# Optimization experiments

Measured on AMD Instinct MI355X. Metric: run time of the kernel, lower is better.

The kernel has to match this reference:

```python
import jax, jax.numpy as jnp
import numpy as np

EPS = 1e-5  # torch LayerNorm default


def setup_inputs() -> dict:
    key = jax.random.key(0)
    ks = jax.random.split(key, 7)
    B, s, i, c, h = 1, 1024, 512, 8, 8
    scale = 0.1
    return {
        "m": jax.random.normal(ks[0], (B, s, i, c), dtype=jnp.float32),
        "ln_gamma": jnp.ones((c,), dtype=jnp.float32),
        "ln_beta": jnp.zeros((c,), dtype=jnp.float32),
        "Wq": jax.random.normal(ks[1], (c * h, c), dtype=jnp.float32) * scale,
        "Wk": jax.random.normal(ks[2], (c, c), dtype=jnp.float32) * scale,
        "Wv": jax.random.normal(ks[3], (c, c), dtype=jnp.float32) * scale,
        "Wg": jax.random.normal(ks[4], (c * h, c), dtype=jnp.float32) * scale,
        "Wo": jax.random.normal(ks[5], (c, c * h), dtype=jnp.float32) * scale,
        "bo": jnp.zeros((c,), dtype=jnp.float32),
    }


def reference(m, ln_gamma, ln_beta, Wq, Wk, Wv, Wg, Wo, bo):
    c = Wk.shape[0]
    h = Wq.shape[0] // c
    B, s, i, _ = m.shape

    # LayerNorm over the channel dim c
    mu = jnp.mean(m, axis=-1, keepdims=True)
    var = jnp.mean(jnp.square(m - mu), axis=-1, keepdims=True)
    x = (m - mu) * jax.lax.rsqrt(var + EPS) * ln_gamma + ln_beta  # (B,s,i,c)

    # projections (torch Linear: y = x @ W.T)
    q = (x @ Wq.T).reshape(B, s, i, h, c).mean(axis=1)            # (B,i,h,c) mean-pooled query
    k = x @ Wk.T                                                   # (B,s,i,c)
    v = x @ Wv.T                                                   # (B,s,i,c)
    gate = jax.nn.sigmoid(x @ Wg.T).reshape(B, s, i, h, c)        # (B,s,i,h,c)

    # attention logits over the column axis t (=s), softmax along t (dim=-3 of b t i h)
    a = jnp.einsum('bihc,btic->btih', q, k) * (c ** -0.5)          # (B,s,i,h)
    a = jax.nn.softmax(a, axis=1)

    o = gate * jnp.einsum('btih,btic->btihc', a, v)               # (B,s,i,h,c)
    o = o.reshape(B, s, i, h * c)
    return o @ Wo.T + bo                                           # (B,s,i,c)
```

## Files before the change

kernel.cpp:

```cpp
#include <hip/hip_runtime.h>

namespace {
constexpr int S = 1024, I = 512, C = 8, H = 8;
constexpr float LNEPS = 1e-5f;
constexpr float SCALE = 0.35355339059327373f;
}

__device__ __forceinline__ float dot8(const float x[8], float4 a, float4 b) {
    float r = x[0] * a.x;
    r += x[1] * a.y; r += x[2] * a.z; r += x[3] * a.w;
    r += x[4] * b.x; r += x[5] * b.y; r += x[6] * b.z; r += x[7] * b.w;
    return r;
}

__device__ __forceinline__ void ln8(float4 a, float4 b, const float gm[8],
                                    const float bt[8], float x[8]) {
    x[0] = a.x; x[1] = a.y; x[2] = a.z; x[3] = a.w;
    x[4] = b.x; x[5] = b.y; x[6] = b.z; x[7] = b.w;
    float mu = 0.f;
#pragma unroll
    for (int c = 0; c < 8; c++) mu += x[c];
    mu *= 0.125f;
    float var = 0.f;
#pragma unroll
    for (int c = 0; c < 8; c++) { float d = x[c] - mu; var += d * d; }
    var *= 0.125f;
    float inv = rsqrtf(var + LNEPS);
#pragma unroll
    for (int c = 0; c < 8; c++) x[c] = (x[c] - mu) * inv * gm[c] + bt[c];
}

__global__ __launch_bounds__(256) void k1_part(const float* __restrict__ m,
                                               const float* __restrict__ gamma,
                                               const float* __restrict__ beta,
                                               float* __restrict__ part1, int CH1) {
    int g = blockIdx.x * 256 + threadIdx.x;
    int i = g & (I - 1);
    int sc = g >> 9;
    int niter = S / CH1;
    float gm[8], bt[8];
#pragma unroll
    for (int c = 0; c < 8; c++) { gm[c] = gamma[c]; bt[c] = beta[c]; }
    float acc[8];
#pragma unroll
    for (int c = 0; c < 8; c++) acc[c] = 0.f;
    const float4* m4 = (const float4*)m;
    for (int j = 0; j < niter; j++) {
        int row = (sc * niter + j) * I + i;
        float x[8];
        ln8(m4[row * 2], m4[row * 2 + 1], gm, bt, x);
#pragma unroll
        for (int c = 0; c < 8; c++) acc[c] += x[c];
    }
    float4* p4 = (float4*)&part1[((size_t)sc * I + i) * 8];
    p4[0] = make_float4(acc[0], acc[1], acc[2], acc[3]);
    p4[1] = make_float4(acc[4], acc[5], acc[6], acc[7]);
}

__global__ __launch_bounds__(64) void k1b_qk(const float* __restrict__ part1,
                                             const float* __restrict__ Wq,
                                             const float* __restrict__ Wk,
                                             float* __restrict__ qk, int CH1) {
    int i = blockIdx.x, t = threadIdx.x;
    float xs[8];
#pragma unroll
    for (int c = 0; c < 8; c++) xs[c] = 0.f;
    const float4* p4 = (const float4*)part1;
    for (int p = t; p < CH1; p += 64) {
        float4 a = p4[((size_t)p * I + i) * 2], b = p4[((size_t)p * I + i) * 2 + 1];
        xs[0] += a.x; xs[1] += a.y; xs[2] += a.z; xs[3] += a.w;
        xs[4] += b.x; xs[5] += b.y; xs[6] += b.z; xs[7] += b.w;
    }
#pragma unroll
    for (int d = 1; d < 64; d <<= 1)
#pragma unroll
        for (int c = 0; c < 8; c++) xs[c] += __shfl_xor(xs[c], d, 64);
    int h = t >> 3, c2 = t & 7;
    float acc = 0.f;
#pragma unroll
    for (int c = 0; c < 8; c++) {
        float qc = 0.f;
#pragma unroll
        for (int c3 = 0; c3 < 8; c3++) qc += xs[c3] * Wq[(h * 8 + c) * 8 + c3];
        acc += qc * Wk[c * 8 + c2];
    }
    qk[i * 64 + t] = acc * (SCALE / 1024.0f);
}

__global__ __launch_bounds__(256) void k2_part(const float* __restrict__ m,
                                               const float* __restrict__ gamma,
                                               const float* __restrict__ beta,
                                               const float* __restrict__ qk,
                                               float* __restrict__ part2, int CH2) {
    int g = blockIdx.x * 256 + threadIdx.x;
    int i = g & (I - 1);
    int sc = g >> 9;
    int niter = S / CH2;
    float gm[8], bt[8];
#pragma unroll
    for (int c = 0; c < 8; c++) { gm[c] = gamma[c]; bt[c] = beta[c]; }
    const float4* qk4 = (const float4*)qk;
    float4 qv[16];
#pragma unroll
    for (int j = 0; j < 16; j++) qv[j] = qk4[i * 16 + j];
    float acc[8];
#pragma unroll
    for (int h = 0; h < 8; h++) acc[h] = 0.f;
    const float4* m4 = (const float4*)m;
    for (int j0 = 0; j0 < niter; j0 += 4) {
        float x[4][8];
#pragma unroll
        for (int r = 0; r < 4; r++) {
            int row = (sc * niter + j0 + r) * I + i;
            ln8(m4[row * 2], m4[row * 2 + 1], gm, bt, x[r]);
        }
#pragma unroll
        for (int h = 0; h < 8; h++)
#pragma unroll
            for (int r = 0; r < 4; r++)
                acc[h] += __expf(dot8(x[r], qv[h * 2], qv[h * 2 + 1]));
    }
    float4* p4 = (float4*)&part2[((size_t)sc * I + i) * 8];
    p4[0] = make_float4(acc[0], acc[1], acc[2], acc[3]);
    p4[1] = make_float4(acc[4], acc[5], acc[6], acc[7]);
}

__global__ __launch_bounds__(64) void k2b_rden(const float* __restrict__ part2,
                                               float* __restrict__ rden, int CH2) {
    int i = blockIdx.x, t = threadIdx.x;
    float d[8];
#pragma unroll
    for (int c = 0; c < 8; c++) d[c] = 0.f;
    const float4* p4 = (const float4*)part2;
    for (int p = t; p < CH2; p += 64) {
        float4 a = p4[((size_t)p * I + i) * 2], b = p4[((size_t)p * I + i) * 2 + 1];
        d[0] += a.x; d[1] += a.y; d[2] += a.z; d[3] += a.w;
        d[4] += b.x; d[5] += b.y; d[6] += b.z; d[7] += b.w;
    }
#pragma unroll
    for (int dd = 1; dd < 64; dd <<= 1)
#pragma unroll
        for (int c = 0; c < 8; c++) d[c] += __shfl_xor(d[c], dd, 64);
    if (t < 8) rden[i * 8 + t] = 1.0f / d[t];
}

__global__ __launch_bounds__(256) void k3_out(const float* __restrict__ m,
                                              const float* __restrict__ gamma,
                                              const float* __restrict__ beta,
                                              const float* __restrict__ Wv,
                                              const float* __restrict__ Wg,
                                              const float* __restrict__ Wo,
                                              const float* __restrict__ bo,
                                              const float* __restrict__ qk,
                                              const float* __restrict__ rden,
                                              float* __restrict__ out) {
    __shared__ __align__(16) float sWv[64];
    __shared__ __align__(16) float sWg[512];
    __shared__ __align__(16) float sWoT[512];
    int t = threadIdx.x;
    if (t < 64) sWv[t] = Wv[t];
    sWg[t] = Wg[t];
    sWg[t + 256] = Wg[t + 256];
    {
        int j = t & 63, c2 = t >> 6;
        sWoT[j * 8 + c2] = Wo[c2 * 64 + j];
        sWoT[j * 8 + c2 + 4] = Wo[(c2 + 4) * 64 + j];
    }
    __syncthreads();

    float gm[8], bt[8], bov[8];
#pragma unroll
    for (int c = 0; c < 8; c++) { gm[c] = gamma[c]; bt[c] = beta[c]; bov[c] = bo[c]; }

    int g = blockIdx.x * 256 + t;
    int i = g & (I - 1);
    int sg = g >> 9;
    const float4* m4 = (const float4*)m;
    float4* out4 = (float4*)out;

    float4 xa[4], xb[4];
#pragma unroll
    for (int r = 0; r < 4; r++) {
        int row = (sg + 256 * r) * I + i;
        xa[r] = m4[row * 2]; xb[r] = m4[row * 2 + 1];
    }
    float x[4][8];
#pragma unroll
    for (int r = 0; r < 4; r++) ln8(xa[r], xb[r], gm, bt, x[r]);

    const float4* sWv4 = (const float4*)sWv;
    const float4* sWg4 = (const float4*)sWg;
    const float4* sWoT4 = (const float4*)sWoT;

    float v[4][8];
#pragma unroll
    for (int c = 0; c < 8; c++) {
        float4 w0 = sWv4[c * 2], w1 = sWv4[c * 2 + 1];
#pragma unroll
        for (int r = 0; r < 4; r++) v[r][c] = dot8(x[r], w0, w1);
    }

    float oacc[4][8];
#pragma unroll
    for (int r = 0; r < 4; r++)
#pragma unroll
        for (int c2 = 0; c2 < 8; c2++) oacc[r][c2] = bov[c2];

    const float4* qk4 = (const float4*)qk;
#pragma unroll 1
    for (int h = 0; h < 8; h++) {
        float4 q0 = qk4[i * 16 + h * 2], q1 = qk4[i * 16 + h * 2 + 1];
        float rd = rden[i * 8 + h];
        float a_[4];
#pragma unroll
        for (int r = 0; r < 4; r++) a_[r] = __expf(dot8(x[r], q0, q1)) * rd;
#pragma unroll
        for (int c = 0; c < 8; c++) {
            int hc = h * 8 + c;
            float4 wg0 = sWg4[hc * 2], wg1 = sWg4[hc * 2 + 1];
            float o_[4];
#pragma unroll
            for (int r = 0; r < 4; r++) {
                float z = dot8(x[r], wg0, wg1);
                float gate = __builtin_amdgcn_rcpf(1.0f + __expf(-z));
                o_[r] = gate * a_[r] * v[r][c];
            }
            float4 wo0 = sWoT4[hc * 2], wo1 = sWoT4[hc * 2 + 1];
#pragma unroll
            for (int r = 0; r < 4; r++) {
                oacc[r][0] += o_[r] * wo0.x; oacc[r][1] += o_[r] * wo0.y;
                oacc[r][2] += o_[r] * wo0.z; oacc[r][3] += o_[r] * wo0.w;
                oacc[r][4] += o_[r] * wo1.x; oacc[r][5] += o_[r] * wo1.y;
                oacc[r][6] += o_[r] * wo1.z; oacc[r][7] += o_[r] * wo1.w;
            }
        }
    }
#pragma unroll
    for (int r = 0; r < 4; r++) {
        int row = (sg + 256 * r) * I + i;
        out4[row * 2] = make_float4(oacc[r][0], oacc[r][1], oacc[r][2], oacc[r][3]);
        out4[row * 2 + 1] = make_float4(oacc[r][4], oacc[r][5], oacc[r][6], oacc[r][7]);
    }
}

extern "C" void kernel_launch(void* const* d_in, const int* in_sizes, int n_in,
                              void* d_out, int out_size, void* d_ws, size_t ws_size,
                              hipStream_t stream) {
    const float* m     = (const float*)d_in[0];
    const float* gamma = (const float*)d_in[1];
    const float* beta  = (const float*)d_in[2];
    const float* Wq    = (const float*)d_in[3];
    const float* Wk    = (const float*)d_in[4];
    const float* Wv    = (const float*)d_in[5];
    const float* Wg    = (const float*)d_in[6];
    const float* Wo    = (const float*)d_in[7];
    const float* bo    = (const float*)d_in[8];
    float* out = (float*)d_out;

    const size_t small = (size_t)I * 64 * 4 + (size_t)I * 8 * 4;
    int CH1 = 256, CH2 = 256;
    auto need = [&](int c1, int c2) {
        return ((size_t)(c1 + c2) * I * C * 4) + small;
    };
    if (need(256, 256) > ws_size) { CH1 = CH2 = 64; }
    if (need(CH1, CH2) > ws_size) { CH1 = CH2 = 16; }

    float* ws    = (float*)d_ws;
    float* part1 = ws;
    float* part2 = part1 + (size_t)CH1 * I * C;
    float* qk    = part2 + (size_t)CH2 * I * C;
    float* rden  = qk + (size_t)I * 64;

    k1_part<<<I * CH1 / 256, 256, 0, stream>>>(m, gamma, beta, part1, CH1);
    k1b_qk<<<I, 64, 0, stream>>>(part1, Wq, Wk, qk, CH1);
    k2_part<<<I * CH2 / 256, 256, 0, stream>>>(m, gamma, beta, qk, part2, CH2);
    k2b_rden<<<I, 64, 0, stream>>>(part2, rden, CH2);
    k3_out<<<I * 256 / 256, 256, 0, stream>>>(m, gamma, beta, Wv, Wg, Wo, bo, qk,
                                              rden, out);
}
```

Baseline: 131.9 us.

## Restructure reductions to coalesced 8-column blocks and double output-kernel grid

The two partial-sum reduction kernels now process 8 columns per 256-thread block. Each wave reads a contiguous 64-float slice per chunk, and the waves combine through shared memory, replacing one 64-thread block per column with strided float4 loads. The output kernel handles 2 rows per thread instead of 4 and launches twice as many blocks with a 4-blocks-per-SM launch bound, aiming for more occupancy and lower register pressure. The chunk count is now a fixed compile-time constant of 256, so the loops fully unroll. The workspace-size fallback is removed, which risks overflow if the workspace is smaller than needed.

```diff
diff --git a/kernel.cpp b/kernel.cpp
--- a/kernel.cpp
+++ b/kernel.cpp
@@ -4,6 +4,7 @@
 constexpr int S = 1024, I = 512, C = 8, H = 8;
 constexpr float LNEPS = 1e-5f;
 constexpr float SCALE = 0.35355339059327373f;
+constexpr int CH = 256;
 }
 
 __device__ __forceinline__ float dot8(const float x[8], float4 a, float4 b) {
@@ -30,14 +31,14 @@
     for (int c = 0; c < 8; c++) x[c] = (x[c] - mu) * inv * gm[c] + bt[c];
 }
 
-__global__ __launch_bounds__(256) void k1_part(const float* __restrict__ m,
-                                               const float* __restrict__ gamma,
-                                               const float* __restrict__ beta,
-                                               float* __restrict__ part1, int CH1) {
+__global__ __launch_bounds__(256) void kA1_part(const float* __restrict__ m,
+                                                const float* __restrict__ gamma,
+                                                const float* __restrict__ beta,
+                                                float* __restrict__ part1) {
     int g = blockIdx.x * 256 + threadIdx.x;
     int i = g & (I - 1);
     int sc = g >> 9;
-    int niter = S / CH1;
+    constexpr int NIT = S / CH;
     float gm[8], bt[8];
 #pragma unroll
     for (int c = 0; c < 8; c++) { gm[c] = gamma[c]; bt[c] = beta[c]; }
@@ -45,8 +46,9 @@
 #pragma unroll
     for (int c = 0; c < 8; c++) acc[c] = 0.f;
     const float4* m4 = (const float4*)m;
-    for (int j = 0; j < niter; j++) {
-        int row = (sc * niter + j) * I + i;
+#pragma unroll
+    for (int j = 0; j < NIT; j++) {
+        int row = (sc * NIT + j) * I + i;
         float x[8];
         ln8(m4[row * 2], m4[row * 2 + 1], gm, bt, x);
 #pragma unroll
@@ -57,45 +59,55 @@
     p4[1] = make_float4(acc[4], acc[5], acc[6], acc[7]);
 }
 
-__global__ __launch_bounds__(64) void k1b_qk(const float* __restrict__ part1,
-                                             const float* __restrict__ Wq,
-                                             const float* __restrict__ Wk,
-                                             float* __restrict__ qk, int CH1) {
-    int i = blockIdx.x, t = threadIdx.x;
-    float xs[8];
-#pragma unroll
-    for (int c = 0; c < 8; c++) xs[c] = 0.f;
-    const float4* p4 = (const float4*)part1;
-    for (int p = t; p < CH1; p += 64) {
-        float4 a = p4[((size_t)p * I + i) * 2], b = p4[((size_t)p * I + i) * 2 + 1];
-        xs[0] += a.x; xs[1] += a.y; xs[2] += a.z; xs[3] += a.w;
-        xs[4] += b.x; xs[5] += b.y; xs[6] += b.z; xs[7] += b.w;
-    }
-#pragma unroll
-    for (int d = 1; d < 64; d <<= 1)
-#pragma unroll
-        for (int c = 0; c < 8; c++) xs[c] += __shfl_xor(xs[c], d, 64);
-    int h = t >> 3, c2 = t & 7;
-    float acc = 0.f;
-#pragma unroll
-    for (int c = 0; c < 8; c++) {
-        float qc = 0.f;
-#pragma unroll
-        for (int c3 = 0; c3 < 8; c3++) qc += xs[c3] * Wq[(h * 8 + c) * 8 + c3];
-        acc += qc * Wk[c * 8 + c2];
-    }
-    qk[i * 64 + t] = acc * (SCALE / 1024.0f);
-}
-
-__global__ __launch_bounds__(256) void k2_part(const float* __restrict__ m,
-                                               const float* __restrict__ gamma,
-                                               const float* __restrict__ beta,
-                                               const float* __restrict__ qk,
-                                               float* __restrict__ part2, int CH2) {
+__global__ __launch_bounds__(256) void kA2_qk(const float* __restrict__ part1,
+                                              const float* __restrict__ Wq,
+                                              const float* __restrict__ Wk,
+                                              float* __restrict__ qk) {
+    __shared__ float red[4][64];
+    __shared__ float xb[64];
+    __shared__ float sWq[512];
+    __shared__ float sWk[64];
+    int t = threadIdx.x;
+    int i0 = blockIdx.x * 8;
+    int w = t >> 6, l = t & 63;
+
+    sWq[t] = Wq[t];
+    sWq[t + 256] = Wq[t + 256];
+    if (t < 64) sWk[t] = Wk[t];
+
+    float sum = 0.f;
+    for (int sc = w; sc < CH; sc += 4)
+        sum += part1[((size_t)sc * I + i0) * 8 + l];
+    red[w][l] = sum;
+    __syncthreads();
+    if (t < 64) xb[t] = red[0][t] + red[1][t] + red[2][t] + red[3][t];
+    __syncthreads();
+
+#pragma unroll
+    for (int o = t; o < 512; o += 256) {
+        int il = o >> 6, hc2 = o & 63, h = hc2 >> 3, c2 = hc2 & 7;
+        float acc = 0.f;
+#pragma unroll
+        for (int c = 0; c < 8; c++) {
+            float q = 0.f;
+#pragma unroll
+            for (int c3 = 0; c3 < 8; c3++)
+                q += xb[il * 8 + c3] * sWq[(h * 8 + c) * 8 + c3];
+            acc += q * sWk[c * 8 + c2];
+        }
+        qk[(i0 + il) * 64 + hc2] = acc * (SCALE / (float)S);
+    }
+}
+
+__global__ __launch_bounds__(256, 4) void kB1_part(const float* __restrict__ m,
+                                                   const float* __restrict__ gamma,
+                                                   const float* __restrict__ beta,
+                                                   const float* __restrict__ qk,
+                                                   float* __restrict__ part2) {
     int g = blockIdx.x * 256 + threadIdx.x;
     int i = g & (I - 1);
     int sc = g >> 9;
-    int niter = S / CH2;
+    constexpr int NIT = S / CH;
     float gm[8], bt[8];
 #pragma unroll
     for (int c = 0; c < 8; c++) { gm[c] = gamma[c]; bt[c] = beta[c]; }
@@ -107,53 +119,45 @@
 #pragma unroll
     for (int h = 0; h < 8; h++) acc[h] = 0.f;
     const float4* m4 = (const float4*)m;
-    for (int j0 = 0; j0 < niter; j0 += 4) {
-        float x[4][8];
-#pragma unroll
-        for (int r = 0; r < 4; r++) {
-            int row = (sc * niter + j0 + r) * I + i;
-            ln8(m4[row * 2], m4[row * 2 + 1], gm, bt, x[r]);
-        }
+#pragma unroll
+    for (int j = 0; j < NIT; j++) {
+        int row = (sc * NIT + j) * I + i;
+        float x[8];
+        ln8(m4[row * 2], m4[row * 2 + 1], gm, bt, x);
 #pragma unroll
         for (int h = 0; h < 8; h++)
-#pragma unroll
-            for (int r = 0; r < 4; r++)
-                acc[h] += __expf(dot8(x[r], qv[h * 2], qv[h * 2 + 1]));
+            acc[h] += __expf(dot8(x, qv[h * 2], qv[h * 2 + 1]));
     }
     float4* p4 = (float4*)&part2[((size_t)sc * I + i) * 8];
     p4[0] = make_float4(acc[0], acc[1], acc[2], acc[3]);
     p4[1] = make_float4(acc[4], acc[5], acc[6], acc[7]);
 }
 
-__global__ __launch_bounds__(64) void k2b_rden(const float* __restrict__ part2,
-                                               float* __restrict__ rden, int CH2) {
-    int i = blockIdx.x, t = threadIdx.x;
-    float d[8];
-#pragma unroll
-    for (int c = 0; c < 8; c++) d[c] = 0.f;
-    const float4* p4 = (const float4*)part2;
-    for (int p = t; p < CH2; p += 64) {
-        float4 a = p4[((size_t)p * I + i) * 2], b = p4[((size_t)p * I + i) * 2 + 1];
-        d[0] += a.x; d[1] += a.y; d[2] += a.z; d[3] += a.w;
-        d[4] += b.x; d[5] += b.y; d[6] += b.z; d[7] += b.w;
-    }
-#pragma unroll
-    for (int dd = 1; dd < 64; dd <<= 1)
-#pragma unroll
-        for (int c = 0; c < 8; c++) d[c] += __shfl_xor(d[c], dd, 64);
-    if (t < 8) rden[i * 8 + t] = 1.0f / d[t];
-}
-
-__global__ __launch_bounds__(256) void k3_out(const float* __restrict__ m,
-                                              const float* __restrict__ gamma,
-                                              const float* __restrict__ beta,
-                                              const float* __restrict__ Wv,
-                                              const float* __restrict__ Wg,
-                                              const float* __restrict__ Wo,
-                                              const float* __restrict__ bo,
-                                              const float* __restrict__ qk,
-                                              const float* __restrict__ rden,
-                                              float* __restrict__ out) {
+__global__ __launch_bounds__(256) void kB2_rden(const float* __restrict__ part2,
+                                                float* __restrict__ rden) {
+    __shared__ float red[4][64];
+    int t = threadIdx.x;
+    int i0 = blockIdx.x * 8;
+    int w = t >> 6, l = t & 63;
+    float sum = 0.f;
+    for (int sc = w; sc < CH; sc += 4)
+        sum += part2[((size_t)sc * I + i0) * 8 + l];
+    red[w][l] = sum;
+    __syncthreads();
+    if (t < 64)
+        rden[i0 * 8 + t] = 1.0f / (red[0][t] + red[1][t] + red[2][t] + red[3][t]);
+}
+
+__global__ __launch_bounds__(256, 4) void kC_out(const float* __restrict__ m,
+                                                 const float* __restrict__ gamma,
+                                                 const float* __restrict__ beta,
+                                                 const float* __restrict__ Wv,
+                                                 const float* __restrict__ Wg,
+                                                 const float* __restrict__ Wo,
+                                                 const float* __restrict__ bo,
+                                                 const float* __restrict__ qk,
+                                                 const float* __restrict__ rden,
+                                                 float* __restrict__ out) {
     __shared__ __align__(16) float sWv[64];
     __shared__ __align__(16) float sWg[512];
     __shared__ __align__(16) float sWoT[512];
@@ -178,31 +182,31 @@
     const float4* m4 = (const float4*)m;
     float4* out4 = (float4*)out;
 
-    float4 xa[4], xb[4];
-#pragma unroll
-    for (int r = 0; r < 4; r++) {
-        int row = (sg + 256 * r) * I + i;
-        xa[r] = m4[row * 2]; xb[r] = m4[row * 2 + 1];
-    }
-    float x[4][8];
-#pragma unroll
-    for (int r = 0; r < 4; r++) ln8(xa[r], xb[r], gm, bt, x[r]);
+    float4 xa[2], xb4[2];
+#pragma unroll
+    for (int r = 0; r < 2; r++) {
+        int row = (sg + 512 * r) * I + i;
+        xa[r] = m4[row * 2]; xb4[r] = m4[row * 2 + 1];
+    }
+    float x[2][8];
+#pragma unroll
+    for (int r = 0; r < 2; r++) ln8(xa[r], xb4[r], gm, bt, x[r]);
 
     const float4* sWv4 = (const float4*)sWv;
     const float4* sWg4 = (const float4*)sWg;
     const float4* sWoT4 = (const float4*)sWoT;
 
-    float v[4][8];
+    float v[2][8];
 #pragma unroll
     for (int c = 0; c < 8; c++) {
         float4 w0 = sWv4[c * 2], w1 = sWv4[c * 2 + 1];
 #pragma unroll
-        for (int r = 0; r < 4; r++) v[r][c] = dot8(x[r], w0, w1);
-    }
-
-    float oacc[4][8];
-#pragma unroll
-    for (int r = 0; r < 4; r++)
+        for (int r = 0; r < 2; r++) v[r][c] = dot8(x[r], w0, w1);
+    }
+
+    float oacc[2][8];
+#pragma unroll
+    for (int r = 0; r < 2; r++)
 #pragma unroll
         for (int c2 = 0; c2 < 8; c2++) oacc[r][c2] = bov[c2];
 
@@ -211,23 +215,23 @@
     for (int h = 0; h < 8; h++) {
         float4 q0 = qk4[i * 16 + h * 2], q1 = qk4[i * 16 + h * 2 + 1];
         float rd = rden[i * 8 + h];
-        float a_[4];
-#pragma unroll
-        for (int r = 0; r < 4; r++) a_[r] = __expf(dot8(x[r], q0, q1)) * rd;
+        float a_[2];
+#pragma unroll
+        for (int r = 0; r < 2; r++) a_[r] = __expf(dot8(x[r], q0, q1)) * rd;
 #pragma unroll
         for (int c = 0; c < 8; c++) {
             int hc = h * 8 + c;
             float4 wg0 = sWg4[hc * 2], wg1 = sWg4[hc * 2 + 1];
-            float o_[4];
-#pragma unroll
-            for (int r = 0; r < 4; r++) {
+            float o_[2];
+#pragma unroll
+            for (int r = 0; r < 2; r++) {
                 float z = dot8(x[r], wg0, wg1);
                 float gate = __builtin_amdgcn_rcpf(1.0f + __expf(-z));
                 o_[r] = gate * a_[r] * v[r][c];
             }
             float4 wo0 = sWoT4[hc * 2], wo1 = sWoT4[hc * 2 + 1];
 #pragma unroll
-            for (int r = 0; r < 4; r++) {
+            for (int r = 0; r < 2; r++) {
                 oacc[r][0] += o_[r] * wo0.x; oacc[r][1] += o_[r] * wo0.y;
                 oacc[r][2] += o_[r] * wo0.z; oacc[r][3] += o_[r] * wo0.w;
                 oacc[r][4] += o_[r] * wo1.x; oacc[r][5] += o_[r] * wo1.y;
@@ -236,8 +240,8 @@
         }
     }
 #pragma unroll
-    for (int r = 0; r < 4; r++) {
-        int row = (sg + 256 * r) * I + i;
+    for (int r = 0; r < 2; r++) {
+        int row = (sg + 512 * r) * I + i;
         out4[row * 2] = make_float4(oacc[r][0], oacc[r][1], oacc[r][2], oacc[r][3]);
         out4[row * 2 + 1] = make_float4(oacc[r][4], oacc[r][5], oacc[r][6], oacc[r][7]);
     }
@@ -257,24 +261,16 @@
     const float* bo    = (const float*)d_in[8];
     float* out = (float*)d_out;
 
-    const size_t small = (size_t)I * 64 * 4 + (size_t)I * 8 * 4;
-    int CH1 = 256, CH2 = 256;
-    auto need = [&](int c1, int c2) {
-        return ((size_t)(c1 + c2) * I * C * 4) + small;
-    };
-    if (need(256, 256) > ws_size) { CH1 = CH2 = 64; }
-    if (need(CH1, CH2) > ws_size) { CH1 = CH2 = 16; }
-
     float* ws    = (float*)d_ws;
     float* part1 = ws;
-    float* part2 = part1 + (size_t)CH1 * I * C;
-    float* qk    = part2 + (size_t)CH2 * I * C;
+    float* part2 = part1 + (size_t)CH * I * C;
+    float* qk    = part2 + (size_t)CH * I * C;
     float* rden  = qk + (size_t)I * 64;
 
-    k1_part<<<I * CH1 / 256, 256, 0, stream>>>(m, gamma, beta, part1, CH1);
-    k1b_qk<<<I, 64, 0, stream>>>(part1, Wq, Wk, qk, CH1);
-    k2_part<<<I * CH2 / 256, 256, 0, stream>>>(m, gamma, beta, qk, part2, CH2);
-    k2b_rden<<<I, 64, 0, stream>>>(part2, rden, CH2);
-    k3_out<<<I * 256 / 256, 256, 0, stream>>>(m, gamma, beta, Wv, Wg, Wo, bo, qk,
-                                              rden, out);
-}
+    kA1_part<<<I * CH / 256, 256, 0, stream>>>(m, gamma, beta, part1);
+    kA2_qk<<<I / 8, 256, 0, stream>>>(part1, Wq, Wk, qk);
+    kB1_part<<<I * CH / 256, 256, 0, stream>>>(m, gamma, beta, qk, part2);
+    kB2_rden<<<I / 8, 256, 0, stream>>>(part2, rden);
+    kC_out<<<I * (S / 2) / 256, 256, 0, stream>>>(m, gamma, beta, Wv, Wg, Wo, bo,
+                                                  qk, rden, out);
+}
```

Measured after the change: 153.9 us. 1.17x slower.
